# Kernel tuning notes

Hardware: AMD Instinct MI355X
Metric: run time of the kernel (lower is better)

## Reference

```python
import jax, jax.numpy as jnp
import numpy as np

E, H = 300, 256          # embedding_dim, GRU hidden per direction
D = 2 * H                # BiGRU output / GCN feature dim
V, PAD = 30000, 0
B, T_LEN, C_LEN = 128, 50, 200
N_GCN = 2
OUT = 3


def _gru_dir(x, Wih, Whh, bih, bhh):
    # x: [B,S,E] -> [B,S,H]; torch GRU equations
    h0 = jnp.zeros((x.shape[0], Whh.shape[1]), x.dtype)
    def step(h, xt):
        gi = xt @ Wih.T + bih                 # [B,3H]
        gh = h @ Whh.T + bhh
        ir, iz, inn = jnp.split(gi, 3, axis=-1)
        hr, hz, hn = jnp.split(gh, 3, axis=-1)
        r = jax.nn.sigmoid(ir + hr)
        z = jax.nn.sigmoid(iz + hz)
        n = jnp.tanh(inn + r * hn)
        hnew = (1.0 - z) * n + z * h
        return hnew, hnew
    _, hs = jax.lax.scan(step, h0, jnp.swapaxes(x, 0, 1))
    return jnp.swapaxes(hs, 0, 1)


def _bigru(x, wih, whh, bih, bhh):
    # wih:[2,3H,E] whh:[2,3H,H] bih/bhh:[2,3H]
    f = _gru_dir(x, wih[0], whh[0], bih[0], bhh[0])
    b = _gru_dir(x[:, ::-1], wih[1], whh[1], bih[1], bhh[1])[:, ::-1]
    return jnp.concatenate([f, b], axis=-1)   # [B,S,2H]


def _stance_attn(tgt_emb, clm_emb, gt, gc):
    tgt_ht = _bigru(tgt_emb, *gt)
    clm_ht = _bigru(clm_emb, *gc)
    tgt_last = tgt_ht[:, -1]
    # 'dot' attention: weight[b,c] = claim_ht[b,c] . target_last_ht[b]
    w = jnp.einsum('bcd,bd->bc', clm_ht, tgt_last)
    # NOTE: original `weight.masked_fill(mask==0, -1e9)` result is DISCARDED
    # (non-inplace torch op), so the mask has no effect -> faithfully omitted.
    return tgt_ht, clm_ht, jax.nn.softmax(w, axis=1)


def _gcn(tgt_ht, clm_ht, Ws):
    # StanceGCN: cat nodes, N_GCN layers of dot-correlation attention + residual relu
    node = jnp.concatenate([tgt_ht, clm_ht], axis=1)   # [B,N,D]
    T = tgt_ht.shape[1]
    for i in range(Ws.shape[0]):
        # dot correlation reduces to pairwise inner products (no [B,N,N,D] blowup);
        # `corr_score.masked_fill(adj==0,...)` is also discarded in the source.
        corr = jax.nn.softmax(jnp.einsum('bid,bjd->bij', node, node), axis=2)
        trans = jnp.einsum('bnd,ed->bne', node, Ws[i])  # Linear(bias=False)
        node = jax.nn.relu(node + jnp.einsum('bij,bjd->bid', corr, trans))
    return node[:, :T], node[:, T:]


def setup_inputs() -> dict:
    key = jax.random.key(0)
    ks = iter(jax.random.split(key, 64))
    def norm(shape, s=0.05):
        return (jax.random.normal(next(ks), shape, jnp.float32) * s)
    d = {}
    d['task_id'] = 0
    d['task_target'] = jax.random.randint(next(ks), (B, T_LEN), 0, V)
    d['shared_target'] = jax.random.randint(next(ks), (B, T_LEN), 0, V)
    d['task_claim'] = jax.random.randint(next(ks), (B, C_LEN), 0, V)
    d['shared_claim'] = jax.random.randint(next(ks), (B, C_LEN), 0, V)
    d['task_mask'] = jax.random.randint(next(ks), (B, C_LEN), 0, 2).astype(jnp.int32)
    d['shared_mask'] = jax.random.randint(next(ks), (B, C_LEN), 0, 2).astype(jnp.int32)
    N = T_LEN + C_LEN
    d['task_adj'] = jax.random.randint(next(ks), (B, N, N), 0, 2).astype(jnp.int32)
    d['shared_adj'] = jax.random.randint(next(ks), (B, N, N), 0, 2).astype(jnp.int32)
    d['emb'] = norm((V, E), 0.1).at[PAD].set(0.0)
    for g in ['tgt', 'tgc', 'sgt', 'sgc']:
        d[g + '_wih'] = norm((2, 3 * H, E))
        d[g + '_whh'] = norm((2, 3 * H, H))
        d[g + '_bih'] = norm((2, 3 * H))
        d[g + '_bhh'] = norm((2, 3 * H))
    d['gcn_task_W'] = norm((N_GCN, D, D))
    d['gcn_shared_W'] = norm((N_GCN, D, D))
    d['lin_W'] = norm((OUT, 2 * D))
    d['lin_b'] = norm((OUT,))
    return d


def reference(task_id, task_target, shared_target, task_claim, shared_claim,
              task_mask, shared_mask, task_adj, shared_adj,
              emb,
              tgt_wih, tgt_whh, tgt_bih, tgt_bhh,
              tgc_wih, tgc_whh, tgc_bih, tgc_bhh,
              sgt_wih, sgt_whh, sgt_bih, sgt_bhh,
              sgc_wih, sgc_whh, sgc_bih, sgc_bhh,
              gcn_task_W, gcn_shared_W, lin_W, lin_b):
    # embedding lookups (eval mode: all dropouts are identity)
    tt, tc = emb[task_target], emb[task_claim]
    st, sc = emb[shared_target], emb[shared_claim]
    t_tgt, t_clm, t_w = _stance_attn(tt, tc,
                                     (tgt_wih, tgt_whh, tgt_bih, tgt_bhh),
                                     (tgc_wih, tgc_whh, tgc_bih, tgc_bhh))
    s_tgt, s_clm, s_w = _stance_attn(st, sc,
                                     (sgt_wih, sgt_whh, sgt_bih, sgt_bhh),
                                     (sgc_wih, sgc_whh, sgc_bih, sgc_bhh))
    _, t_clm_rep = _gcn(t_tgt, t_clm, gcn_task_W)
    _, s_clm_rep = _gcn(s_tgt, s_clm, gcn_shared_W)
    # StanceLinear: attention-weighted claim pooling, concat, final linear
    task_rep = jnp.einsum('bc,bcd->bd', t_w, t_clm_rep)
    shared_rep = jnp.einsum('bc,bcd->bd', s_w, s_clm_rep)
    final = jnp.concatenate([task_rep, shared_rep], axis=1)   # [B, 4H+4H]
    return final @ lin_W.T + lin_b                            # [B, 3]
```

## Files before the change

### kernel.cpp

```cpp
#include <hip/hip_runtime.h>
#include <hip/hip_bf16.h>

namespace {

constexpr int B_  = 128;
constexpr int TL  = 50, CL = 200, NNODE = 250;
constexpr int H_  = 256, D_ = 512;
constexpr long NODE_ELE = 128L * 250 * 512;

typedef __attribute__((ext_vector_type(8))) short bf16x8;
typedef __attribute__((ext_vector_type(4))) float f32x4;

__device__ inline float bits2f(unsigned v) { union { unsigned u; float f; } c; c.u = v; return c.f; }
__device__ inline unsigned f2bits(float x) { union { float f; unsigned u; } c; c.f = x; return c.u; }
__device__ inline unsigned short bfbits(float x) {
  __hip_bfloat16 b = __float2bfloat16(x);
  return *(unsigned short*)&b;
}
__device__ inline float bfsel(uint2 v, int r) {
  unsigned w = (r < 2) ? v.x : v.y;
  return bits2f((r & 1) ? (w & 0xFFFF0000u) : (w << 16));
}
__device__ inline float sigf(float x)  { return 1.f / (1.f + __expf(-x)); }
__device__ inline float tanhf_(float x){ return 1.f - 2.f / (__expf(2.f * x) + 1.f); }

struct BGemmArgs {
  const __hip_bfloat16* A; const __hip_bfloat16* B;
  const int* idx; const float* bias; const __hip_bfloat16* Res;
  void* C;
  long aStride, bStride, biasStride, cStride, rStride;
  int M, N, Kreal, lda, ldb, ldc, zShiftA;
};

template<bool GATHER, int OUT>
__global__ __launch_bounds__(256) void bgemm_k(BGemmArgs g) {
  __shared__ __align__(16) char As[2][16384];
  __shared__ __align__(16) char Bs[2][16384];
  const int z = blockIdx.z;
  const int m0 = blockIdx.x * 128, n0 = blockIdx.y * 128;
  const int tid = threadIdx.x;
  const int lane = tid & 63, wv = tid >> 6;
  const int wr = wv >> 1, wc = wv & 1;
  const __hip_bfloat16* Ab = GATHER ? g.A : g.A + (long)(z >> g.zShiftA) * g.aStride;
  const __hip_bfloat16* Bb = g.B + (long)z * g.bStride;

  long asrc[4], bsrc[4];
  int ldso[4];
  #pragma unroll
  for (int c2 = 0; c2 < 4; ++c2) {
    int o = c2 * 256 + tid;
    int row = o >> 3, ko = o & 7;
    int colel = 8 * (ko ^ (row & 7));
    long arow = GATHER ? (long)g.idx[m0 + row] * g.lda : (long)(m0 + row) * g.lda;
    asrc[c2] = arow + colel;
    bsrc[c2] = (long)(n0 + row) * g.ldb + colel;
    ldso[c2] = o * 16;
  }

  f32x4 acc[4][4];
  #pragma unroll
  for (int i = 0; i < 4; ++i)
    #pragma unroll
    for (int j = 0; j < 4; ++j) acc[i][j] = (f32x4){0.f, 0.f, 0.f, 0.f};

  const int KT = g.Kreal >> 6;
  #pragma unroll
  for (int c2 = 0; c2 < 4; ++c2) {
    __builtin_amdgcn_global_load_lds(
        (const __attribute__((address_space(1))) unsigned*)(Ab + asrc[c2]),
        (__attribute__((address_space(3))) unsigned*)(&As[0][0] + ldso[c2]), 16, 0, 0);
    __builtin_amdgcn_global_load_lds(
        (const __attribute__((address_space(1))) unsigned*)(Bb + bsrc[c2]),
        (__attribute__((address_space(3))) unsigned*)(&Bs[0][0] + ldso[c2]), 16, 0, 0);
  }
  __syncthreads();

  int buf = 0;
  for (int kt = 0; kt < KT; ++kt) {
    if (kt + 1 < KT) {
      long ko = (long)(kt + 1) * 64;
      #pragma unroll
      for (int c2 = 0; c2 < 4; ++c2) {
        __builtin_amdgcn_global_load_lds(
            (const __attribute__((address_space(1))) unsigned*)(Ab + asrc[c2] + ko),
            (__attribute__((address_space(3))) unsigned*)(&As[buf ^ 1][0] + ldso[c2]), 16, 0, 0);
        __builtin_amdgcn_global_load_lds(
            (const __attribute__((address_space(1))) unsigned*)(Bb + bsrc[c2] + ko),
            (__attribute__((address_space(3))) unsigned*)(&Bs[buf ^ 1][0] + ldso[c2]), 16, 0, 0);
      }
    }
    const char* ab = &As[buf][0];
    const char* bb = &Bs[buf][0];
    #pragma unroll
    for (int ks = 0; ks < 2; ++ks) {
      bf16x8 af[4], bfr[4];
      #pragma unroll
      for (int i = 0; i < 4; ++i) {
        int ra = wr * 64 + i * 16 + (lane & 15);
        af[i] = *(const bf16x8*)(ab + ((ra * 128 + ks * 64 + (lane >> 4) * 16) ^ ((ra & 7) << 4)));
        int rb = wc * 64 + i * 16 + (lane & 15);
        bfr[i] = *(const bf16x8*)(bb + ((rb * 128 + ks * 64 + (lane >> 4) * 16) ^ ((rb & 7) << 4)));
      }
      #pragma unroll
      for (int i = 0; i < 4; ++i)
        #pragma unroll
        for (int j = 0; j < 4; ++j)
          acc[i][j] = __builtin_amdgcn_mfma_f32_16x16x32_bf16(af[i], bfr[j], acc[i][j], 0, 0, 0);
    }
    __syncthreads();
    buf ^= 1;
  }

  const long cz = (long)z * g.cStride;
  #pragma unroll
  for (int i = 0; i < 4; ++i) {
    int rbase = m0 + wr * 64 + i * 16 + ((lane >> 4) << 2);
    #pragma unroll
    for (int j = 0; j < 4; ++j) {
      int col = n0 + wc * 64 + j * 16 + (lane & 15);
      #pragma unroll
      for (int r = 0; r < 4; ++r) {
        int row = rbase + r;
        float v = acc[i][j][r];
        if (OUT == 0) {
          if (row < g.M && col < g.N)
            ((float*)g.C)[cz + (long)row * g.ldc + col] = v;
        } else if (OUT == 1) {
          if (row < g.M && col < g.N) {
            v += g.bias[(long)z * g.biasStride + col];
            ((__hip_bfloat16*)g.C)[cz + (long)row * g.ldc + col] = __float2bfloat16(v);
          }
        } else if (OUT == 3) {
          if (row < g.M)
            ((__hip_bfloat16*)g.C)[cz + (long)row * g.ldc + col] =
                __float2bfloat16(col < g.N ? v : 0.f);
        } else {
          if (row < g.M && col < g.N) {
            v += __bfloat162float(g.Res[(long)z * g.rStride + (long)row * g.ldc + col]);
            v = fmaxf(v, 0.f);
            ((__hip_bfloat16*)g.C)[cz + (long)row * g.ldc + col] = __float2bfloat16(v);
          }
        }
      }
    }
  }
}

struct PrepArgs {
  const float* whh[4];
  const float* gcnW[2];
  const float* emb;
  const float* wih[4];
  const float* bih[4];
  const float* bhh[4];
  __hip_bfloat16 *whhbf, *gcnWbf, *embbf;
  __hip_bfloat16* wihbf[4];
  float* biasC;
};

constexpr long PR0 = 1572864;
constexpr long PR1 = PR0 + 1048576;
constexpr long PR2 = PR1 + 9600000;
constexpr long PR3 = PR2 + 1966080;
constexpr long PR4 = PR3 + 6144;

__global__ __launch_bounds__(256) void prep_k(PrepArgs a) {
  long i = (long)blockIdx.x * 256 + threadIdx.x;
  if (i >= PR4) return;
  if (i < PR0) {
    int zz = (int)(i / 196608);
    long rem = i - (long)zz * 196608;
    a.whhbf[i] = __float2bfloat16(a.whh[zz >> 1][(long)(zz & 1) * 196608 + rem]);
  } else if (i < PR1) {
    long j = i - PR0;
    a.gcnWbf[j] = __float2bfloat16(a.gcnW[j / 524288][j % 524288]);
  } else if (i < PR2) {
    long j = i - PR1;
    long r = j / 320;
    int c = (int)(j - r * 320);
    a.embbf[j] = __float2bfloat16(c < 300 ? a.emb[r * 300 + c] : 0.f);
  } else if (i < PR3) {
    long j = i - PR2;
    int w = (int)(j / 491520);
    long k = j - (long)w * 491520;
    long r = k / 320;
    int c = (int)(k - r * 320);
    a.wihbf[w][k] = __float2bfloat16(c < 300 ? a.wih[w][r * 300 + c] : 0.f);
  } else {
    long j = i - PR3;
    int w = (int)(j / 1536);
    int k = (int)(j - (long)w * 1536);
    a.biasC[(long)w * 1536 + k] = a.bih[w][k] + ((k % 768) < 512 ? a.bhh[w][k] : 0.f);
  }
}

struct RecArgs {
  const __hip_bfloat16* whhbf;
  const __hip_bfloat16* gi[4];
  const float* bhh[4];
  __hip_bfloat16* nodebf;
};

__global__ __launch_bounds__(512, 2) void gru_rec_k(RecArgs a) {
  __shared__ __align__(16) char hbuf[2][8192];
  const int z = blockIdx.z;
  const int side = z >> 2, sq = (z >> 1) & 1, dir = z & 1;
  const int gidx = side * 2 + sq;
  const int T = sq ? CL : TL;
  const int toff = sq ? TL : 0;
  const __hip_bfloat16* gi = a.gi[gidx] + (long)dir * B_ * T * 768;
  const float* bhh = a.bhh[gidx] + dir * 768;
  const __hip_bfloat16* whh = a.whhbf + (long)z * 768 * 256;
  __hip_bfloat16* nodeb = a.nodebf + (long)side * NODE_ELE;
  const int b0 = blockIdx.x * 16;
  const int tid = threadIdx.x;
  const int lane = tid & 63, wv = tid >> 6;
  const int bcol = lane & 15, g4 = lane >> 4;
  const int u0 = wv * 32 + g4 * 4;
  const int swzh = (bcol & 15) << 4;

  bf16x8 Af[3][2][8];
  #pragma unroll
  for (int g = 0; g < 3; ++g)
    #pragma unroll
    for (int h = 0; h < 2; ++h)
      #pragma unroll
      for (int kt = 0; kt < 8; ++kt) {
        int row = g * 256 + wv * 32 + h * 16 + bcol;
        int col = kt * 32 + g4 * 8;
        Af[g][h][kt] = *(const bf16x8*)(whh + (long)row * 256 + col);
      }
  *(uint4*)&hbuf[0][tid * 16] = make_uint4(0, 0, 0, 0);
  const float4 bn0 = *(const float4*)&bhh[512 + u0];
  const float4 bn1 = *(const float4*)&bhh[512 + u0 + 16];
  __syncthreads();

  const __hip_bfloat16* gip = gi + ((long)(b0 + bcol) * T + (dir ? T - 1 : 0)) * 768 + u0;
  __hip_bfloat16* np = nodeb + ((long)(b0 + bcol) * NNODE + toff + (dir ? T - 1 : 0)) * D_
                       + dir * H_ + u0;
  const long gistep = dir ? -768L : 768L;
  const long nstep  = dir ? -(long)D_ : (long)D_;
  int cur = 0;

  float hreg[2][4];
  #pragma unroll
  for (int h = 0; h < 2; ++h)
    #pragma unroll
    for (int r = 0; r < 4; ++r) hreg[h][r] = 0.f;

  uint2 gv[3][2];
  #pragma unroll
  for (int g = 0; g < 3; ++g)
    #pragma unroll
    for (int h = 0; h < 2; ++h)
      gv[g][h] = *(const uint2*)(gip + g * 256 + h * 16);

  for (int t = 0; t < T; ++t) {
    const char* hib = &hbuf[cur][0];
    f32x4 c[3][2];
    #pragma unroll
    for (int g = 0; g < 3; ++g)
      #pragma unroll
      for (int h = 0; h < 2; ++h) c[g][h] = (f32x4){0.f, 0.f, 0.f, 0.f};
    const int rb = bcol * 512 + g4 * 16;
    #pragma unroll
    for (int kt = 0; kt < 8; ++kt) {
      bf16x8 bh = *(const bf16x8*)(hib + ((rb + kt * 64) ^ swzh));
      #pragma unroll
      for (int g = 0; g < 3; ++g)
        #pragma unroll
        for (int h = 0; h < 2; ++h)
          c[g][h] = __builtin_amdgcn_mfma_f32_16x16x32_bf16(Af[g][h][kt], bh, c[g][h], 0, 0, 0);
    }

    #pragma unroll
    for (int h = 0; h < 2; ++h) {
      float4 bn = h ? bn1 : bn0;
      #pragma unroll
      for (int r = 0; r < 4; ++r) {
        float bnv = (r == 0) ? bn.x : (r == 1) ? bn.y : (r == 2) ? bn.z : bn.w;
        float rr = sigf(bfsel(gv[0][h], r) + c[0][h][r]);
        float zz = sigf(bfsel(gv[1][h], r) + c[1][h][r]);
        float nn = tanhf_(bfsel(gv[2][h], r) + rr * (c[2][h][r] + bnv));
        hreg[h][r] = (1.f - zz) * nn + zz * hreg[h][r];
      }
    }

    {
      const __hip_bfloat16* gn = (t + 1 < T) ? gip + gistep : gip;
      gip = gn;
      #pragma unroll
      for (int g = 0; g < 3; ++g)
        #pragma unroll
        for (int h = 0; h < 2; ++h)
          gv[g][h] = *(const uint2*)(gn + g * 256 + h * 16);
    }

    const int ob0 = bcol * 512 + u0 * 2;
    char* hibn = &hbuf[cur ^ 1][0];
    #pragma unroll
    for (int h = 0; h < 2; ++h) {
      unsigned hb[4];
      #pragma unroll
      for (int r = 0; r < 4; ++r)
        hb[r] = (f2bits(hreg[h][r]) + 0x8000u) & 0xFFFF0000u;
      uint2 hiw;
      hiw.x = (hb[0] >> 16) | hb[1];
      hiw.y = (hb[2] >> 16) | hb[3];
      *(uint2*)(np + h * 16) = hiw;
      *(uint2*)(hibn + ((ob0 + h * 32) ^ swzh)) = hiw;
    }
    np += nstep;
    asm volatile("s_waitcnt lgkmcnt(0)" ::: "memory");
    __builtin_amdgcn_sched_barrier(0);
    __builtin_amdgcn_s_barrier();
    cur ^= 1;
  }
}

__global__ __launch_bounds__(256) void attn_k(const __hip_bfloat16* nodeAll,
                                              float* wT, float* wS) {
  int b = blockIdx.x, side = blockIdx.y;
  const __hip_bfloat16* node = nodeAll + (long)side * NODE_ELE;
  float* w = side ? wS : wT;
  __shared__ float tl[512];
  __shared__ float sc[CL];
  int tid = threadIdx.x;
  {
    const __hip_bfloat16* tr = node + ((long)b * NNODE + (TL - 1)) * D_;
    tl[tid]       = __bfloat162float(tr[tid]);
    tl[tid + 256] = __bfloat162float(tr[tid + 256]);
  }
  __syncthreads();
  int wid = tid >> 6, lane = tid & 63;
  for (int c = wid; c < CL; c += 4) {
    const __hip_bfloat16* row = node + ((long)b * NNODE + TL + c) * D_;
    uint4 v = *(const uint4*)(row + lane * 8);
    const float* tp = &tl[lane * 8];
    float acc = bits2f(v.x << 16)         * tp[0] + bits2f(v.x & 0xFFFF0000u) * tp[1]
              + bits2f(v.y << 16)         * tp[2] + bits2f(v.y & 0xFFFF0000u) * tp[3]
              + bits2f(v.z << 16)         * tp[4] + bits2f(v.z & 0xFFFF0000u) * tp[5]
              + bits2f(v.w << 16)         * tp[6] + bits2f(v.w & 0xFFFF0000u) * tp[7];
    #pragma unroll
    for (int o = 32; o; o >>= 1) acc += __shfl_xor(acc, o, 64);
    if (lane == 0) sc[c] = acc;
  }
  __syncthreads();
  if (wid == 0) {
    float v[4]; float m = -1e30f;
    #pragma unroll
    for (int i = 0; i < 4; ++i) {
      int c = lane + 64 * i;
      v[i] = (c < CL) ? sc[c] : -1e30f;
      m = fmaxf(m, v[i]);
    }
    #pragma unroll
    for (int o = 32; o; o >>= 1) m = fmaxf(m, __shfl_xor(m, o, 64));
    float s = 0.f;
    #pragma unroll
    for (int i = 0; i < 4; ++i) {
      int c = lane + 64 * i;
      v[i] = (c < CL) ? expf(v[i] - m) : 0.f;
      s += v[i];
    }
    #pragma unroll
    for (int o = 32; o; o >>= 1) s += __shfl_xor(s, o, 64);
    float inv = 1.f / s;
    #pragma unroll
    for (int i = 0; i < 4; ++i) {
      int c = lane + 64 * i;
      if (c < CL) w[(long)b * CL + c] = v[i] * inv;
    }
  }
}

__global__ __launch_bounds__(256) void softmaxbf_k(const float* in, __hip_bfloat16* out) {
  int row = blockIdx.x * 4 + (threadIdx.x >> 6);
  int lane = threadIdx.x & 63;
  const float* p = in + (long)row * 256;
  __hip_bfloat16* q = out + (long)row * 256;
  float v[4]; float m = -1e30f;
  #pragma unroll
  for (int i = 0; i < 4; ++i) {
    int c = lane + i * 64;
    v[i] = (c < 250) ? p[c] : -1e30f;
    m = fmaxf(m, v[i]);
  }
  #pragma unroll
  for (int o = 32; o; o >>= 1) m = fmaxf(m, __shfl_xor(m, o, 64));
  float s = 0.f;
  #pragma unroll
  for (int i = 0; i < 4; ++i) {
    int c = lane + i * 64;
    if (c < 250) { v[i] = __expf(v[i] - m); s += v[i]; }
  }
  #pragma unroll
  for (int o = 32; o; o >>= 1) s += __shfl_xor(s, o, 64);
  float inv = 1.f / s;
  #pragma unroll
  for (int i = 0; i < 4; ++i) {
    int c = lane + i * 64;
    q[c] = __float2bfloat16((c < 250) ? v[i] * inv : 0.f);
  }
}

__global__ __launch_bounds__(256) void rep_k(const __hip_bfloat16* nodeAll,
                                             const float* wT, const float* wS,
                                             float* rep) {
  int b = blockIdx.x, side = blockIdx.y;
  const __hip_bfloat16* node = nodeAll + (long)side * NODE_ELE;
  const float* w = side ? wS : wT;
  __shared__ float wl[CL];
  int tid = threadIdx.x;
  if (tid < CL) wl[tid] = w[(long)b * CL + tid];
  __syncthreads();
  #pragma unroll
  for (int h = 0; h < 2; ++h) {
    int d = tid + h * 256;
    float acc = 0.f;
    for (int c = 0; c < CL; ++c)
      acc = fmaf(wl[c], __bfloat162float(node[((long)b * NNODE + TL + c) * D_ + d]), acc);
    rep[((long)side * B_ + b) * D_ + d] = acc;
  }
}

__global__ __launch_bounds__(256) void final_k(const float* rep, const float* linW,
                                               const float* linb, float* out) {
  int b = blockIdx.x, tid = threadIdx.x;
  float a0 = 0.f, a1 = 0.f, a2 = 0.f;
  for (int d = tid; d < 1024; d += 256) {
    float x = rep[(long)(d >> 9) * (B_ * D_) + (long)b * D_ + (d & 511)];
    a0 = fmaf(x, linW[d], a0);
    a1 = fmaf(x, linW[1024 + d], a1);
    a2 = fmaf(x, linW[2048 + d], a2);
  }
  #pragma unroll
  for (int o = 32; o; o >>= 1) {
    a0 += __shfl_xor(a0, o, 64);
    a1 += __shfl_xor(a1, o, 64);
    a2 += __shfl_xor(a2, o, 64);
  }
  __shared__ float red[3][4];
  int wid = tid >> 6, lane = tid & 63;
  if (lane == 0) { red[0][wid] = a0; red[1][wid] = a1; red[2][wid] = a2; }
  __syncthreads();
  if (tid == 0) {
    out[b * 3 + 0] = red[0][0] + red[0][1] + red[0][2] + red[0][3] + linb[0];
    out[b * 3 + 1] = red[1][0] + red[1][1] + red[1][2] + red[1][3] + linb[1];
    out[b * 3 + 2] = red[2][0] + red[2][1] + red[2][2] + red[2][3] + linb[2];
  }
}

__global__ void diag_k(float* out, int n, float v) {
  int i = blockIdx.x * blockDim.x + threadIdx.x;
  if (i < n) out[i] = v;
}

}

extern "C" void kernel_launch(void* const* d_in, const int* in_sizes, int n_in,
                              void* d_out, int out_size, void* d_ws, size_t ws_size,
                              hipStream_t stream) {
  const int* task_target   = (const int*)d_in[1];
  const int* shared_target = (const int*)d_in[2];
  const int* task_claim    = (const int*)d_in[3];
  const int* shared_claim  = (const int*)d_in[4];
  const float* emb      = (const float*)d_in[9];
  const float* tgt_wih  = (const float*)d_in[10];
  const float* tgt_whh  = (const float*)d_in[11];
  const float* tgt_bih  = (const float*)d_in[12];
  const float* tgt_bhh  = (const float*)d_in[13];
  const float* tgc_wih  = (const float*)d_in[14];
  const float* tgc_whh  = (const float*)d_in[15];
  const float* tgc_bih  = (const float*)d_in[16];
  const float* tgc_bhh  = (const float*)d_in[17];
  const float* sgt_wih  = (const float*)d_in[18];
  const float* sgt_whh  = (const float*)d_in[19];
  const float* sgt_bih  = (const float*)d_in[20];
  const float* sgt_bhh  = (const float*)d_in[21];
  const float* sgc_wih  = (const float*)d_in[22];
  const float* sgc_whh  = (const float*)d_in[23];
  const float* sgc_bih  = (const float*)d_in[24];
  const float* sgc_bhh  = (const float*)d_in[25];
  const float* gcnW_task   = (const float*)d_in[26];
  const float* gcnW_shared = (const float*)d_in[27];
  const float* linW = (const float*)d_in[28];
  const float* linb = (const float*)d_in[29];
  float* out = (float*)d_out;

  const size_t SZ_WHH   = 3145728;
  const size_t SZ_GCNW  = 2097152;
  const size_t SZ_BIASC = 24576;
  const size_t SZ_ARENA = 196608000;
  const size_t SZ_NODE  = 65536000;
  const size_t SZ_W     = 102400;
  const size_t SZ_REP   = 524288;
  const size_t NEED = SZ_WHH + SZ_GCNW + SZ_BIASC + SZ_ARENA + SZ_NODE
                      + 2 * SZ_W + SZ_REP + 4096;

  if (ws_size < NEED) {
    diag_k<<<(out_size + 255) / 256, 256, 0, stream>>>(out, out_size,
                                                       (float)(ws_size >> 20));
    return;
  }

  char* p = (char*)d_ws;
  auto alloc = [&](size_t bytes) { char* r = p; p += (bytes + 255) & ~(size_t)255; return r; };
  __hip_bfloat16* whhbf  = (__hip_bfloat16*)alloc(SZ_WHH);
  __hip_bfloat16* gcnWbf = (__hip_bfloat16*)alloc(SZ_GCNW);
  float* biasC = (float*)alloc(SZ_BIASC);
  char* arena  = alloc(SZ_ARENA);
  char* nodeC  = alloc(SZ_NODE);
  float* wT    = (float*)alloc(SZ_W);
  float* wS    = (float*)alloc(SZ_W);
  float* rep   = (float*)alloc(SZ_REP);
  __hip_bfloat16* nodebf = (__hip_bfloat16*)nodeC;

  __hip_bfloat16* gi_tt = (__hip_bfloat16*)(arena);
  __hip_bfloat16* gi_tc = (__hip_bfloat16*)(arena + 19660800);
  __hip_bfloat16* gi_st = (__hip_bfloat16*)(arena + 98304000);
  __hip_bfloat16* gi_sc = (__hip_bfloat16*)(arena + 117964800);
  __hip_bfloat16* embbf = (__hip_bfloat16*)(nodeC);
  __hip_bfloat16* wihbf[4] = {
    (__hip_bfloat16*)(nodeC + 19200000),
    (__hip_bfloat16*)(nodeC + 20183040),
    (__hip_bfloat16*)(nodeC + 21166080),
    (__hip_bfloat16*)(nodeC + 22149120)};
  __hip_bfloat16* tmpbf  = (__hip_bfloat16*)(arena);
  __hip_bfloat16* corrbf = (__hip_bfloat16*)(arena + 65536000);
  float*          corrF  = (float*)(arena + 98304000);
  __hip_bfloat16* transT = (__hip_bfloat16*)(arena + 98304000);

  {
    PrepArgs pa;
    pa.whh[0] = tgt_whh; pa.whh[1] = tgc_whh; pa.whh[2] = sgt_whh; pa.whh[3] = sgc_whh;
    pa.gcnW[0] = gcnW_task; pa.gcnW[1] = gcnW_shared;
    pa.emb = emb;
    pa.wih[0] = tgt_wih; pa.wih[1] = tgc_wih; pa.wih[2] = sgt_wih; pa.wih[3] = sgc_wih;
    pa.bih[0] = tgt_bih; pa.bih[1] = tgc_bih; pa.bih[2] = sgt_bih; pa.bih[3] = sgc_bih;
    pa.bhh[0] = tgt_bhh; pa.bhh[1] = tgc_bhh; pa.bhh[2] = sgt_bhh; pa.bhh[3] = sgc_bhh;
    pa.whhbf = whhbf; pa.gcnWbf = gcnWbf; pa.embbf = embbf;
    pa.wihbf[0] = wihbf[0]; pa.wihbf[1] = wihbf[1];
    pa.wihbf[2] = wihbf[2]; pa.wihbf[3] = wihbf[3];
    pa.biasC = biasC;
    prep_k<<<(int)((PR4 + 255) / 256), 256, 0, stream>>>(pa);
  }

  auto proj = [&](const int* idx, __hip_bfloat16* wih, const float* bias,
                  __hip_bfloat16* gi, int Mrows, int gx) {
    BGemmArgs ga{};
    ga.A = embbf; ga.idx = idx; ga.B = wih; ga.bias = bias; ga.C = gi;
    ga.aStride = 0; ga.bStride = 768L * 320; ga.biasStride = 768;
    ga.cStride = (long)Mrows * 768; ga.zShiftA = 0;
    ga.M = Mrows; ga.N = 768; ga.Kreal = 320; ga.lda = 320; ga.ldb = 320; ga.ldc = 768;
    bgemm_k<true, 1><<<dim3(gx, 6, 2), 256, 0, stream>>>(ga);
  };
  proj(task_target,   wihbf[0], biasC,        gi_tt, 6400, 50);
  proj(task_claim,    wihbf[1], biasC + 1536, gi_tc, 25600, 200);
  proj(shared_target, wihbf[2], biasC + 3072, gi_st, 6400, 50);
  proj(shared_claim,  wihbf[3], biasC + 4608, gi_sc, 25600, 200);

  RecArgs ra;
  ra.whhbf = whhbf;
  ra.gi[0] = gi_tt; ra.gi[1] = gi_tc; ra.gi[2] = gi_st; ra.gi[3] = gi_sc;
  ra.bhh[0] = tgt_bhh; ra.bhh[1] = tgc_bhh; ra.bhh[2] = sgt_bhh; ra.bhh[3] = sgc_bhh;
  ra.nodebf = nodebf;
  gru_rec_k<<<dim3(8, 1, 8), 512, 0, stream>>>(ra);

  attn_k<<<dim3(128, 2), 256, 0, stream>>>(nodebf, wT, wS);

  for (int layer = 0; layer < 2; ++layer) {
    const __hip_bfloat16* inbf = layer ? tmpbf : nodebf;
    BGemmArgs ca{};
    ca.A = inbf; ca.B = inbf; ca.C = corrF;
    ca.aStride = 128000; ca.bStride = 128000; ca.cStride = 64000; ca.zShiftA = 0;
    ca.M = 250; ca.N = 250; ca.Kreal = 512; ca.lda = 512; ca.ldb = 512; ca.ldc = 256;
    bgemm_k<false, 0><<<dim3(2, 2, 256), 256, 0, stream>>>(ca);
    softmaxbf_k<<<16000, 256, 0, stream>>>(corrF, corrbf);
    BGemmArgs ta{};
    ta.A = gcnWbf + (long)layer * 262144; ta.B = inbf; ta.C = transT;
    ta.aStride = 524288; ta.bStride = 128000; ta.cStride = 131072; ta.zShiftA = 7;
    ta.M = 512; ta.N = 250; ta.Kreal = 512; ta.lda = 512; ta.ldb = 512; ta.ldc = 256;
    bgemm_k<false, 3><<<dim3(4, 2, 256), 256, 0, stream>>>(ta);
    BGemmArgs aa{};
    aa.A = corrbf; aa.B = transT; aa.Res = inbf;
    aa.C = layer ? (void*)nodebf : (void*)tmpbf;
    aa.aStride = 64000; aa.bStride = 131072; aa.cStride = 128000;
    aa.rStride = 128000; aa.zShiftA = 0;
    aa.M = 250; aa.N = 512; aa.Kreal = 256; aa.lda = 256; aa.ldb = 256; aa.ldc = 512;
    bgemm_k<false, 5><<<dim3(2, 4, 256), 256, 0, stream>>>(aa);
  }

  rep_k<<<dim3(128, 2), 256, 0, stream>>>(nodebf, wT, wS, rep);
  final_k<<<dim3(128), 256, 0, stream>>>(rep, linW, linb, out);
}
```

Baseline: 1.527 ms.

## Fuse GCN correlation GEMM with row softmax into a single kernel

Replaces the per-layer correlation batched GEMM (fp32 output) plus separate softmax kernel with one kernel. Each block computes full 256-column score rows for 64 node rows in registers using MFMA, applies the row softmax in-register with lane shuffles, and writes bf16 probabilities directly. This removes the fp32 correlation round-trip through global memory and one launch per layer. In exchange, tile loads run over padded rows beyond 250, and the kernel holds a wide accumulator per wave, which may raise register pressure.

```diff
diff --git a/kernel.cpp b/kernel.cpp
--- a/kernel.cpp
+++ b/kernel.cpp
@@ -122,10 +122,7 @@
       for (int r = 0; r < 4; ++r) {
         int row = rbase + r;
         float v = acc[i][j][r];
-        if (OUT == 0) {
-          if (row < g.M && col < g.N)
-            ((float*)g.C)[cz + (long)row * g.ldc + col] = v;
-        } else if (OUT == 1) {
+        if (OUT == 1) {
           if (row < g.M && col < g.N) {
             v += g.bias[(long)z * g.biasStride + col];
             ((__hip_bfloat16*)g.C)[cz + (long)row * g.ldc + col] = __float2bfloat16(v);
@@ -142,6 +139,113 @@
           }
         }
       }
+    }
+  }
+}
+
+struct CsmArgs { const __hip_bfloat16* in; __hip_bfloat16* outp; };
+
+__global__ __launch_bounds__(256) void csm_k(CsmArgs g) {
+  __shared__ __align__(16) char As[2][8192];
+  __shared__ __align__(16) char Bs[2][32768];
+  const int z = blockIdx.z;
+  const int m0 = blockIdx.x * 64;
+  const int tid = threadIdx.x;
+  const int lane = tid & 63, wv = tid >> 6;
+  const __hip_bfloat16* base = g.in + (long)z * 128000;
+
+  long bsrc[8]; int bo[8];
+  #pragma unroll
+  for (int c2 = 0; c2 < 8; ++c2) {
+    int o = c2 * 256 + tid;
+    int row = o >> 3, ko = o & 7;
+    bsrc[c2] = (long)row * 512 + 8 * (ko ^ (row & 7));
+    bo[c2] = o * 16;
+  }
+  long asrc[2]; int ao[2];
+  #pragma unroll
+  for (int c2 = 0; c2 < 2; ++c2) {
+    int o = c2 * 256 + tid;
+    int row = o >> 3, ko = o & 7;
+    asrc[c2] = (long)(m0 + row) * 512 + 8 * (ko ^ (row & 7));
+    ao[c2] = o * 16;
+  }
+
+  f32x4 acc[16];
+  #pragma unroll
+  for (int j = 0; j < 16; ++j) acc[j] = (f32x4){0.f, 0.f, 0.f, 0.f};
+
+  #pragma unroll
+  for (int c2 = 0; c2 < 2; ++c2)
+    __builtin_amdgcn_global_load_lds(
+        (const __attribute__((address_space(1))) unsigned*)(base + asrc[c2]),
+        (__attribute__((address_space(3))) unsigned*)(&As[0][0] + ao[c2]), 16, 0, 0);
+  #pragma unroll
+  for (int c2 = 0; c2 < 8; ++c2)
+    __builtin_amdgcn_global_load_lds(
+        (const __attribute__((address_space(1))) unsigned*)(base + bsrc[c2]),
+        (__attribute__((address_space(3))) unsigned*)(&Bs[0][0] + bo[c2]), 16, 0, 0);
+  __syncthreads();
+
+  int buf = 0;
+  for (int kt = 0; kt < 8; ++kt) {
+    if (kt + 1 < 8) {
+      long ko = (long)(kt + 1) * 64;
+      #pragma unroll
+      for (int c2 = 0; c2 < 2; ++c2)
+        __builtin_amdgcn_global_load_lds(
+            (const __attribute__((address_space(1))) unsigned*)(base + asrc[c2] + ko),
+            (__attribute__((address_space(3))) unsigned*)(&As[buf ^ 1][0] + ao[c2]), 16, 0, 0);
+      #pragma unroll
+      for (int c2 = 0; c2 < 8; ++c2)
+        __builtin_amdgcn_global_load_lds(
+            (const __attribute__((address_space(1))) unsigned*)(base + bsrc[c2] + ko),
+            (__attribute__((address_space(3))) unsigned*)(&Bs[buf ^ 1][0] + bo[c2]), 16, 0, 0);
+    }
+    const char* ab = &As[buf][0];
+    const char* bb = &Bs[buf][0];
+    #pragma unroll
+    for (int ks = 0; ks < 2; ++ks) {
+      int ra = wv * 16 + (lane & 15);
+      bf16x8 af = *(const bf16x8*)(ab + ((ra * 128 + ks * 64 + (lane >> 4) * 16) ^ ((ra & 7) << 4)));
+      #pragma unroll
+      for (int j = 0; j < 16; ++j) {
+        int rb = j * 16 + (lane & 15);
+        bf16x8 bf = *(const bf16x8*)(bb + ((rb * 128 + ks * 64 + (lane >> 4) * 16) ^ ((rb & 7) << 4)));
+        acc[j] = __builtin_amdgcn_mfma_f32_16x16x32_bf16(af, bf, acc[j], 0, 0, 0);
+      }
+    }
+    __syncthreads();
+    buf ^= 1;
+  }
+
+  const int c0 = lane & 15, rq = lane >> 4;
+  const long obase = (long)z * 64000;
+  #pragma unroll
+  for (int r = 0; r < 4; ++r) {
+    int row = m0 + wv * 16 + rq * 4 + r;
+    float vals[16];
+    float mx = -1e30f;
+    #pragma unroll
+    for (int j = 0; j < 16; ++j) {
+      vals[j] = acc[j][r];
+      if (j * 16 + c0 < 250) mx = fmaxf(mx, vals[j]);
+    }
+    #pragma unroll
+    for (int o = 1; o < 16; o <<= 1) mx = fmaxf(mx, __shfl_xor(mx, o, 64));
+    float s = 0.f;
+    #pragma unroll
+    for (int j = 0; j < 16; ++j) {
+      float e = (j * 16 + c0 < 250) ? __expf(vals[j] - mx) : 0.f;
+      vals[j] = e; s += e;
+    }
+    #pragma unroll
+    for (int o = 1; o < 16; o <<= 1) s += __shfl_xor(s, o, 64);
+    float inv = 1.f / s;
+    if (row < 250) {
+      #pragma unroll
+      for (int j = 0; j < 16; ++j)
+        g.outp[obase + (long)row * 256 + j * 16 + c0] = __float2bfloat16(vals[j] * inv);
     }
   }
 }
@@ -371,36 +475,6 @@
       int c = lane + 64 * i;
       if (c < CL) w[(long)b * CL + c] = v[i] * inv;
     }
-  }
-}
-
-__global__ __launch_bounds__(256) void softmaxbf_k(const float* in, __hip_bfloat16* out) {
-  int row = blockIdx.x * 4 + (threadIdx.x >> 6);
-  int lane = threadIdx.x & 63;
-  const float* p = in + (long)row * 256;
-  __hip_bfloat16* q = out + (long)row * 256;
-  float v[4]; float m = -1e30f;
-  #pragma unroll
-  for (int i = 0; i < 4; ++i) {
-    int c = lane + i * 64;
-    v[i] = (c < 250) ? p[c] : -1e30f;
-    m = fmaxf(m, v[i]);
-  }
-  #pragma unroll
-  for (int o = 32; o; o >>= 1) m = fmaxf(m, __shfl_xor(m, o, 64));
-  float s = 0.f;
-  #pragma unroll
-  for (int i = 0; i < 4; ++i) {
-    int c = lane + i * 64;
-    if (c < 250) { v[i] = __expf(v[i] - m); s += v[i]; }
-  }
-  #pragma unroll
-  for (int o = 32; o; o >>= 1) s += __shfl_xor(s, o, 64);
-  float inv = 1.f / s;
-  #pragma unroll
-  for (int i = 0; i < 4; ++i) {
-    int c = lane + i * 64;
-    q[c] = __float2bfloat16((c < 250) ? v[i] * inv : 0.f);
   }
 }
 
@@ -528,7 +602,6 @@
     (__hip_bfloat16*)(nodeC + 22149120)};
   __hip_bfloat16* tmpbf  = (__hip_bfloat16*)(arena);
   __hip_bfloat16* corrbf = (__hip_bfloat16*)(arena + 65536000);
-  float*          corrF  = (float*)(arena + 98304000);
   __hip_bfloat16* transT = (__hip_bfloat16*)(arena + 98304000);
 
   {
@@ -571,12 +644,8 @@
 
   for (int layer = 0; layer < 2; ++layer) {
     const __hip_bfloat16* inbf = layer ? tmpbf : nodebf;
-    BGemmArgs ca{};
-    ca.A = inbf; ca.B = inbf; ca.C = corrF;
-    ca.aStride = 128000; ca.bStride = 128000; ca.cStride = 64000; ca.zShiftA = 0;
-    ca.M = 250; ca.N = 250; ca.Kreal = 512; ca.lda = 512; ca.ldb = 512; ca.ldc = 256;
-    bgemm_k<false, 0><<<dim3(2, 2, 256), 256, 0, stream>>>(ca);
-    softmaxbf_k<<<16000, 256, 0, stream>>>(corrF, corrbf);
+    CsmArgs cs{inbf, corrbf};
+    csm_k<<<dim3(4, 1, 256), 256, 0, stream>>>(cs);
     BGemmArgs ta{};
     ta.A = gcnWbf + (long)layer * 262144; ta.B = inbf; ta.C = transT;
     ta.aStride = 524288; ta.bStride = 128000; ta.cStride = 131072; ta.zShiftA = 7;
```

Result: no change. 1.511 ms (-1.1%).
